# Kernel tuning notes

Measured on AMD Instinct MI355X. Metric: run time of the kernel, lower is better.

The kernel has to match this reference:

```python
import jax, jax.numpy as jnp
import numpy as np

B, T = 8, 4096
H, V, K = 512, 32000, 9


def setup_inputs() -> dict:
    key = jax.random.key(0)
    k1, k2, k3 = jax.random.split(key, 3)
    x = jax.random.randint(k1, (B, T), 0, V, dtype=jnp.int32)
    # conv1d weight [out_ch=H, in_ch=V, K], xavier-like scale
    scale = 1.0 / np.sqrt(V * K)
    W = jax.random.normal(k2, (H, V, K), dtype=jnp.float32) * scale
    b = jax.random.normal(k3, (H,), dtype=jnp.float32) * 0.01
    return {"x": x, "W": W, "b": b}


def reference(x, W, b):
    """one_hot(x, V) -> conv1d(V->H, K, pad=K//2) expressed as gather+sum.

    out[b,t,c] = bias[c] + sum_k W[c, x[b, t+k-pad], k]  (zero outside [0,T)).
    """
    Bx, Tx = x.shape
    Hh, Vv, Kk = W.shape
    pad = Kk // 2
    t = jnp.arange(Tx)
    acc = jnp.zeros((Bx, Tx, Hh), dtype=W.dtype)
    for k in range(Kk):  # small fixed kernel loop (K=9)
        src = t + (k - pad)                      # [T]
        valid = (src >= 0) & (src < Tx)          # [T]
        src_c = jnp.clip(src, 0, Tx - 1)
        ids = x[:, src_c]                        # [B,T]
        emb = jnp.take(W[:, :, k].T, ids, axis=0)  # [B,T,H] gather of column k
        acc = acc + jnp.where(valid[None, :, None], emb, jnp.zeros((), W.dtype))
    return acc + b  # [B,T,H]
```

## Files before the change

kernel.cpp:

```cpp
#include <hip/hip_runtime.h>
#include <hip/hip_bf16.h>


#define Hc 512
#define Vc 32000
#define Kc 9
#define Tc 4096
#define Bc 8
#define Mc (Vc * Kc)
#define ROWU ((Kc * Hc) / 2)
#define T_TILE 32
#define WT_ROWS (Vc + 1)

__device__ __forceinline__ unsigned short f2bf(float f) {
  unsigned int u = __float_as_uint(f);
  u += 0x7FFFu + ((u >> 16) & 1u);
  return (unsigned short)(u >> 16);
}

__global__ __launch_bounds__(256) void mark_kernel(
    const int* __restrict__ x, int* __restrict__ slot, int* __restrict__ counter) {
  const int i = blockIdx.x * 256 + threadIdx.x;
  const int v = x[i];
  if (atomicCAS(&slot[v], -1, -2147483647) == -1) {
    slot[v] = 1 + atomicAdd(counter, 1);
  }
}

__global__ __launch_bounds__(256) void wt_transpose_kernel(
    const float* __restrict__ in, unsigned int* __restrict__ outu,
    const int* __restrict__ slot) {
  __shared__ float tile[64][65];
  const int m0 = blockIdx.x * 64;
  const int c0 = blockIdx.y * 64;
  const int tx = threadIdx.x & 63;
  const int ty = threadIdx.x >> 6;
#pragma unroll
  for (int r = 0; r < 16; ++r) {
    const int row = ty * 16 + r;
    tile[row][tx] = in[(size_t)(c0 + row) * Mc + (m0 + tx)];
  }
  __syncthreads();
  const int u = threadIdx.x & 31;
  const int rl = threadIdx.x >> 5;
#pragma unroll
  for (int p = 0; p < 8; ++p) {
    const int mrow = p * 8 + rl;
    const int m = m0 + mrow;
    const int v = m / Kc;
    const int k = m - v * Kc;
    const int s = slot[v];
    if (s >= 0) {
      const unsigned int val = (unsigned int)f2bf(tile[2 * u][mrow]) |
                               ((unsigned int)f2bf(tile[2 * u + 1][mrow]) << 16);
      outu[(size_t)s * ROWU + k * (Hc / 2) + (c0 >> 1) + u] = val;
    }
  }
}

__global__ __launch_bounds__(256) void conv_gather_kernel(
    const int* __restrict__ x, const unsigned int* __restrict__ Wt,
    const int* __restrict__ slot, const float* __restrict__ bias,
    float* __restrict__ out) {
  __shared__ int ids[T_TILE + Kc - 1];
  const int blk = blockIdx.x;
  const int b = blk >> 7;
  const int t0 = (blk & 127) * T_TILE;
  const int tid = threadIdx.x;
  if (tid < T_TILE + Kc - 1) {
    const int s = t0 + tid - (Kc / 2);
    ids[tid] = (s >= 0 && s < Tc) ? slot[x[b * Tc + s]] : 0;
  }
  __syncthreads();
  const float2 b2 = *(const float2*)(bias + 2 * tid);
  float2* out2 = (float2*)out;
  for (int tt = 0; tt < T_TILE; ++tt) {
    float2 acc = b2;
#pragma unroll
    for (int k = 0; k < Kc; ++k) {
      const int id = ids[tt + k];
      const unsigned int w = Wt[(size_t)id * ROWU + k * (Hc / 2) + tid];
      acc.x += __uint_as_float(w << 16);
      acc.y += __uint_as_float(w & 0xFFFF0000u);
    }
    out2[(size_t)(b * Tc + t0 + tt) * (Hc / 2) + tid] = acc;
  }
}

__global__ __launch_bounds__(256) void conv_fallback_kernel(
    const int* __restrict__ x, const float* __restrict__ W,
    const float* __restrict__ bias, float* __restrict__ out) {
  const size_t idx = (size_t)blockIdx.x * 256 + threadIdx.x;
  const int c = (int)(idx & (Hc - 1));
  const size_t bt = idx >> 9;
  const int t = (int)(bt & (Tc - 1));
  const int b = (int)(bt >> 12);
  float acc = bias[c];
#pragma unroll
  for (int k = 0; k < Kc; ++k) {
    const int s = t + k - (Kc / 2);
    if (s >= 0 && s < Tc) {
      const int id = x[b * Tc + s];
      acc += W[(size_t)c * Mc + (size_t)id * Kc + k];
    }
  }
  out[idx] = acc;
}

extern "C" void kernel_launch(void* const* d_in, const int* in_sizes, int n_in,
                              void* d_out, int out_size, void* d_ws, size_t ws_size,
                              hipStream_t stream) {
  const int* x = (const int*)d_in[0];
  const float* W = (const float*)d_in[1];
  const float* bias = (const float*)d_in[2];
  float* out = (float*)d_out;

  const size_t wt_bytes = (size_t)WT_ROWS * ROWU * 4;
  const size_t slot_off = wt_bytes;
  const size_t cnt_off = slot_off + (size_t)Vc * 4;
  const size_t need = cnt_off + 4;

  if (ws_size >= need) {
    unsigned int* Wt = (unsigned int*)d_ws;
    int* slot = (int*)((char*)d_ws + slot_off);
    int* counter = (int*)((char*)d_ws + cnt_off);
    hipMemsetAsync(slot, 0xFF, (size_t)Vc * 4, stream);
    hipMemsetAsync(counter, 0, 4, stream);
    hipMemsetAsync(Wt, 0, (size_t)Kc * Hc * 2, stream);
    mark_kernel<<<(Bc * Tc) / 256, 256, 0, stream>>>(x, slot, counter);
    dim3 g1(Mc / 64, Hc / 64);
    wt_transpose_kernel<<<g1, 256, 0, stream>>>(W, Wt, slot);
    conv_gather_kernel<<<Bc * (Tc / T_TILE), 256, 0, stream>>>(
        x, Wt, slot, bias, out);
  } else {
    const size_t n = (size_t)Bc * Tc * Hc;
    conv_fallback_kernel<<<(int)(n / 256), 256, 0, stream>>>(x, W, bias, out);
  }
}
```

Baseline: 234.8 us.

## Pipeline weight transpose and gather across channel chunks in one fused kernel

Splits the output channels into four chunks of 128 and launches a fused kernel five times. Within each launch, most blocks transpose and convert the next chunk of W to bf16 into one of two ping-pong buffers, while every tenth block gathers and sums the previous chunk. The goal is to overlap the bandwidth-heavy transpose with the gather and to shrink the per-chunk staging table so it stays cache-resident. In exchange it adds launches, a second workspace buffer, idle early-return blocks in the first and last launches, and narrower 64-lane writes per gather row.

```diff
diff --git a/kernel.cpp b/kernel.cpp
--- a/kernel.cpp
+++ b/kernel.cpp
@@ -8,9 +8,13 @@
 #define Tc 4096
 #define Bc 8
 #define Mc (Vc * Kc)
-#define ROWU ((Kc * Hc) / 2)
+#define CHUNK_C 128
+#define NCHUNK 4
+#define ROW_U (Kc * CHUNK_C / 2)
+#define WT_ROWS (Vc + 1)
 #define T_TILE 32
-#define WT_ROWS (Vc + 1)
+#define NTB 9000
+#define NGB 1024
 
 __device__ __forceinline__ unsigned short f2bf(float f) {
   unsigned int u = __float_as_uint(f);
@@ -27,63 +31,77 @@
   }
 }
 
-__global__ __launch_bounds__(256) void wt_transpose_kernel(
-    const float* __restrict__ in, unsigned int* __restrict__ outu,
-    const int* __restrict__ slot) {
+__global__ __launch_bounds__(256) void fused_kernel(
+    const float* __restrict__ W, const int* __restrict__ x,
+    const int* __restrict__ slot, const float* __restrict__ bias,
+    float* __restrict__ out, unsigned int* __restrict__ wbuf,
+    const unsigned int* __restrict__ rbuf, int tchunk, int gchunk) {
   __shared__ float tile[64][65];
-  const int m0 = blockIdx.x * 64;
-  const int c0 = blockIdx.y * 64;
-  const int tx = threadIdx.x & 63;
-  const int ty = threadIdx.x >> 6;
+  const int bx = blockIdx.x;
+  const int rem = bx % 10;
+  const int tid = threadIdx.x;
+
+  if (rem != 9) {
+    if (tchunk >= NCHUNK) return;
+    const int tb = (bx / 10) * 9 + rem;
+    if (tb >= NTB) return;
+    const int mt = tb % 4500;
+    const int ct = tb / 4500;
+    const int m0 = mt * 64;
+    const int cbase = tchunk * CHUNK_C + ct * 64;
+    const int tx = tid & 63;
+    const int ty = tid >> 6;
 #pragma unroll
-  for (int r = 0; r < 16; ++r) {
-    const int row = ty * 16 + r;
-    tile[row][tx] = in[(size_t)(c0 + row) * Mc + (m0 + tx)];
-  }
-  __syncthreads();
-  const int u = threadIdx.x & 31;
-  const int rl = threadIdx.x >> 5;
+    for (int r = 0; r < 16; ++r) {
+      const int row = ty * 16 + r;
+      tile[row][tx] = W[(size_t)(cbase + row) * Mc + (m0 + tx)];
+    }
+    __syncthreads();
+    const int u = tid & 31;
+    const int rl = tid >> 5;
 #pragma unroll
-  for (int p = 0; p < 8; ++p) {
-    const int mrow = p * 8 + rl;
-    const int m = m0 + mrow;
-    const int v = m / Kc;
-    const int k = m - v * Kc;
-    const int s = slot[v];
-    if (s >= 0) {
-      const unsigned int val = (unsigned int)f2bf(tile[2 * u][mrow]) |
-                               ((unsigned int)f2bf(tile[2 * u + 1][mrow]) << 16);
-      outu[(size_t)s * ROWU + k * (Hc / 2) + (c0 >> 1) + u] = val;
+    for (int p = 0; p < 8; ++p) {
+      const int mrow = p * 8 + rl;
+      const int m = m0 + mrow;
+      const int v = m / Kc;
+      const int k = m - v * Kc;
+      const int s = slot[v];
+      if (s >= 0) {
+        const unsigned int val =
+            (unsigned int)f2bf(tile[2 * u][mrow]) |
+            ((unsigned int)f2bf(tile[2 * u + 1][mrow]) << 16);
+        wbuf[(size_t)s * ROW_U + k * (CHUNK_C / 2) + ct * 32 + u] = val;
+      }
     }
-  }
-}
-
-__global__ __launch_bounds__(256) void conv_gather_kernel(
-    const int* __restrict__ x, const unsigned int* __restrict__ Wt,
-    const int* __restrict__ slot, const float* __restrict__ bias,
-    float* __restrict__ out) {
-  __shared__ int ids[T_TILE + Kc - 1];
-  const int blk = blockIdx.x;
-  const int b = blk >> 7;
-  const int t0 = (blk & 127) * T_TILE;
-  const int tid = threadIdx.x;
-  if (tid < T_TILE + Kc - 1) {
-    const int s = t0 + tid - (Kc / 2);
-    ids[tid] = (s >= 0 && s < Tc) ? slot[x[b * Tc + s]] : 0;
-  }
-  __syncthreads();
-  const float2 b2 = *(const float2*)(bias + 2 * tid);
-  float2* out2 = (float2*)out;
-  for (int tt = 0; tt < T_TILE; ++tt) {
-    float2 acc = b2;
+  } else {
+    if (gchunk < 0) return;
+    const int gb = bx / 10;
+    int* ids = (int*)tile;
+    const int b = gb >> 7;
+    const int t0 = (gb & 127) * T_TILE;
+    if (tid < T_TILE + Kc - 1) {
+      const int s = t0 + tid - (Kc / 2);
+      ids[tid] = (s >= 0 && s < Tc) ? slot[x[b * Tc + s]] : 0;
+    }
+    __syncthreads();
+    const int lane = tid & 63;
+    const int w = tid >> 6;
+    const int c0 = gchunk * CHUNK_C;
+    const int cpair = c0 + 2 * lane;
+    const float2 b2 = *(const float2*)(bias + cpair);
 #pragma unroll
-    for (int k = 0; k < Kc; ++k) {
-      const int id = ids[tt + k];
-      const unsigned int w = Wt[(size_t)id * ROWU + k * (Hc / 2) + tid];
-      acc.x += __uint_as_float(w << 16);
-      acc.y += __uint_as_float(w & 0xFFFF0000u);
+    for (int i = 0; i < 8; ++i) {
+      const int tt = w * 8 + i;
+      float2 acc = b2;
+#pragma unroll
+      for (int k = 0; k < Kc; ++k) {
+        const int id = ids[tt + k];
+        const unsigned int wv = rbuf[(size_t)id * ROW_U + k * (CHUNK_C / 2) + lane];
+        acc.x += __uint_as_float(wv << 16);
+        acc.y += __uint_as_float(wv & 0xFFFF0000u);
+      }
+      *(float2*)(out + ((size_t)(b * Tc + t0 + tt) << 9) + cpair) = acc;
     }
-    out2[(size_t)(b * Tc + t0 + tt) * (Hc / 2) + tid] = acc;
   }
 }
 
@@ -115,23 +133,31 @@
   const float* bias = (const float*)d_in[2];
   float* out = (float*)d_out;
 
-  const size_t wt_bytes = (size_t)WT_ROWS * ROWU * 4;
-  const size_t slot_off = wt_bytes;
+  const size_t buf_bytes = (size_t)WT_ROWS * ROW_U * 4;
+  const size_t buf1_off = buf_bytes;
+  const size_t slot_off = 2 * buf_bytes;
   const size_t cnt_off = slot_off + (size_t)Vc * 4;
   const size_t need = cnt_off + 4;
 
   if (ws_size >= need) {
-    unsigned int* Wt = (unsigned int*)d_ws;
+    unsigned int* buf0 = (unsigned int*)d_ws;
+    unsigned int* buf1 = (unsigned int*)((char*)d_ws + buf1_off);
     int* slot = (int*)((char*)d_ws + slot_off);
     int* counter = (int*)((char*)d_ws + cnt_off);
     hipMemsetAsync(slot, 0xFF, (size_t)Vc * 4, stream);
     hipMemsetAsync(counter, 0, 4, stream);
-    hipMemsetAsync(Wt, 0, (size_t)Kc * Hc * 2, stream);
+    hipMemsetAsync(buf0, 0, ROW_U * 4, stream);
+    hipMemsetAsync(buf1, 0, ROW_U * 4, stream);
     mark_kernel<<<(Bc * Tc) / 256, 256, 0, stream>>>(x, slot, counter);
-    dim3 g1(Mc / 64, Hc / 64);
-    wt_transpose_kernel<<<g1, 256, 0, stream>>>(W, Wt, slot);
-    conv_gather_kernel<<<Bc * (Tc / T_TILE), 256, 0, stream>>>(
-        x, Wt, slot, bias, out);
+    const int grid = 10240;
+    for (int l = 0; l <= NCHUNK; ++l) {
+      const int tchunk = l;
+      const int gchunk = l - 1;
+      unsigned int* wbuf = (tchunk & 1) ? buf1 : buf0;
+      const unsigned int* rbuf = (gchunk >= 0 && (gchunk & 1)) ? buf1 : buf0;
+      fused_kernel<<<grid, 256, 0, stream>>>(W, x, slot, bias, out, wbuf, rbuf,
+                                             tchunk, gchunk);
+    }
   } else {
     const size_t n = (size_t)Bc * Tc * Hc;
     conv_fallback_kernel<<<(int)(n / 256), 256, 0, stream>>>(x, W, bias, out);
```

Result: slower. 244.4 us (+4.1%).
